# Kernel tuning notes

Hardware: AMD Instinct MI355X
Metric: run time of the kernel (lower is better)

Reference implementation:

```python
import jax, jax.numpy as jnp
import numpy as np
from jax import lax

START_IDX = 7
STOP_IDX = 8
TAGSET = 9
VOCAB = 50257
EMB = 512
HID = 1024  # bidirectional: HID//2 per direction
SEQ = 8192


def _lstm_dir(x, Wih, Whh, bih, bhh, reverse):
    # x: [T, EMB]; Wih: [4H, EMB]; Whh: [4H, H]
    H = Whh.shape[1]
    xproj = x @ Wih.T + bih  # big GEMM hoisted out of the scan: [T, 4H]

    def step(carry, xp):
        h, c = carry
        g = xp + h @ Whh.T + bhh
        i, f, gg, o = jnp.split(g, 4)
        i = jax.nn.sigmoid(i)
        f = jax.nn.sigmoid(f)
        gg = jnp.tanh(gg)
        o = jax.nn.sigmoid(o)
        c = f * c + i * gg
        h = o * jnp.tanh(c)
        return (h, c), h

    init = (jnp.zeros((H,), x.dtype), jnp.zeros((H,), x.dtype))
    _, hs = lax.scan(step, init, xproj, reverse=reverse)
    return hs  # [T, H]


def _viterbi(feats, transitions):
    # feats: [T, TAGSET]; transitions[next, prev]
    init = jnp.full((TAGSET,), -10000.0, feats.dtype).at[START_IDX].set(0.0)

    def step(fv, feat):
        scores = fv[None, :] + transitions       # [next, prev]
        bp = jnp.argmax(scores, axis=1)          # best prev per next tag
        fv_new = jnp.max(scores, axis=1) + feat
        return fv_new, bp

    fv, bptrs = lax.scan(step, init, feats)
    terminal = fv + transitions[STOP_IDX]
    best = jnp.argmax(terminal)
    path_score = terminal[best]

    def back(c, bp):
        return bp[c], c

    _, path = lax.scan(back, best, bptrs, reverse=True)  # path[t] = tag at t
    return path_score, path.astype(jnp.int32)


def setup_inputs() -> dict:
    key = jax.random.key(0)
    ks = jax.random.split(key, 13)
    H = HID // 2
    s = lambda *sh: 0.05
    inp = {
        'sentence': jax.random.randint(ks[0], (SEQ,), 0, VOCAB, dtype=jnp.int32),
        'emb': jax.random.normal(ks[1], (VOCAB + 100, EMB), jnp.float32) * 0.05,
        'Wih_f': jax.random.normal(ks[2], (4 * H, EMB), jnp.float32) * 0.05,
        'Whh_f': jax.random.normal(ks[3], (4 * H, H), jnp.float32) * 0.05,
        'bih_f': jnp.zeros((4 * H,), jnp.float32),
        'bhh_f': jnp.zeros((4 * H,), jnp.float32),
        'Wih_b': jax.random.normal(ks[4], (4 * H, EMB), jnp.float32) * 0.05,
        'Whh_b': jax.random.normal(ks[5], (4 * H, H), jnp.float32) * 0.05,
        'bih_b': jnp.zeros((4 * H,), jnp.float32),
        'bhh_b': jnp.zeros((4 * H,), jnp.float32),
        'W_out': jax.random.normal(ks[6], (TAGSET, HID), jnp.float32) * 0.05,
        'b_out': jnp.zeros((TAGSET,), jnp.float32),
    }
    trans = jax.random.normal(ks[7], (TAGSET, TAGSET), jnp.float32)
    trans = trans.at[START_IDX, :].set(-10000.0)
    trans = trans.at[:, STOP_IDX].set(-10000.0)
    inp['transitions'] = trans
    return inp


def reference(sentence, emb, Wih_f, Whh_f, bih_f, bhh_f, Wih_b, Whh_b, bih_b, bhh_b, W_out, b_out, transitions):
    x = emb[sentence]                                   # [T, EMB]
    h_f = _lstm_dir(x, Wih_f, Whh_f, bih_f, bhh_f, reverse=False)
    h_b = _lstm_dir(x, Wih_b, Whh_b, bih_b, bhh_b, reverse=True)
    lstm_out = jnp.concatenate([h_f, h_b], axis=-1)     # [T, HID]
    feats = lstm_out @ W_out.T + b_out                  # [T, TAGSET]
    score, path = _viterbi(feats, transitions)
    return score, path
```

## Files before the change

kernel.cpp:

```cpp
#include <hip/hip_runtime.h>
#include <hip/hip_bf16.h>


#define T_SEQ   8192
#define EMB     512
#define HDIM    512
#define POISON64 0x7F7F7F7F7F7F7F7Full

#define ALOAD(p)  __hip_atomic_load((p), __ATOMIC_RELAXED, __HIP_MEMORY_SCOPE_AGENT)

__global__ __launch_bounds__(256) void gemm_xproj(
    const int* __restrict__ sentence, const float* __restrict__ emb,
    const float* __restrict__ Wih_f, const float* __restrict__ Wih_b,
    const float* __restrict__ bih_f, const float* __restrict__ bhh_f,
    const float* __restrict__ bih_b, const float* __restrict__ bhh_b,
    float* __restrict__ xprojb)
{
    __shared__ float As[16][132];
    __shared__ float Bs[16][132];
    __shared__ int   srow[128];

    const int tid = threadIdx.x;
    const int bm = blockIdx.x;
    const int bn = blockIdx.y;
    const int fwd = (bn < 16);
    const float* __restrict__ W = fwd ? Wih_f : Wih_b;
    const int jbase = bn * 128 - (fwd ? 0 : 2048);

    if (tid < 128) srow[tid] = sentence[bm * 128 + tid];
    __syncthreads();

    const int lkk = tid & 15;
    const int lr  = tid >> 4;
    int sr[8];
    #pragma unroll
    for (int i = 0; i < 8; ++i) sr[i] = srow[lr * 8 + i];
    const float* wbase = W + (size_t)(jbase + lr * 8) * EMB + lkk;

    const int tx = tid & 15, ty = tid >> 4;
    float acc[8][8] = {};

    for (int kb = 0; kb < 32; ++kb) {
        const int k0 = kb * 16;
        #pragma unroll
        for (int i = 0; i < 8; ++i) {
            As[lkk][lr * 8 + i] = emb[(size_t)sr[i] * EMB + k0 + lkk];
            Bs[lkk][lr * 8 + i] = wbase[(size_t)i * EMB + k0];
        }
        __syncthreads();
        #pragma unroll
        for (int kk = 0; kk < 16; ++kk) {
            const float4 a0 = *(const float4*)&As[kk][ty * 8];
            const float4 a1 = *(const float4*)&As[kk][ty * 8 + 4];
            const float4 b0 = *(const float4*)&Bs[kk][tx * 8];
            const float4 b1 = *(const float4*)&Bs[kk][tx * 8 + 4];
            const float av[8] = {a0.x,a0.y,a0.z,a0.w,a1.x,a1.y,a1.z,a1.w};
            const float bv[8] = {b0.x,b0.y,b0.z,b0.w,b1.x,b1.y,b1.z,b1.w};
            #pragma unroll
            for (int i = 0; i < 8; ++i)
                #pragma unroll
                for (int j = 0; j < 8; ++j)
                    acc[i][j] = fmaf(av[i], bv[j], acc[i][j]);
        }
        __syncthreads();
    }

    const float* b1p = fwd ? bih_f : bih_b;
    const float* b2p = fwd ? bhh_f : bhh_b;
    float bias[8];
    #pragma unroll
    for (int j = 0; j < 8; ++j) {
        const int jj = jbase + tx * 8 + j;
        bias[j] = b1p[jj] + b2p[jj];
    }
    #pragma unroll
    for (int i = 0; i < 8; ++i) {
        const int t = bm * 128 + ty * 8 + i;
        float4* dst = (float4*)&xprojb[(size_t)t * 4096 + bn * 128 + tx * 8];
        dst[0] = make_float4(acc[i][0] + bias[0], acc[i][1] + bias[1],
                             acc[i][2] + bias[2], acc[i][3] + bias[3]);
        dst[1] = make_float4(acc[i][4] + bias[4], acc[i][5] + bias[5],
                             acc[i][6] + bias[6], acc[i][7] + bias[7]);
    }
}

__device__ __forceinline__ float fsig(float x) { return 1.0f / (1.0f + __expf(-x)); }
__device__ __forceinline__ float ftanh(float x) {
    const float e = __expf(-2.0f * fabsf(x));
    return copysignf((1.0f - e) / (1.0f + e), x);
}
__device__ __forceinline__ unsigned long long pack2(float a, float b) {
    return (unsigned long long)__float_as_uint(a) |
           ((unsigned long long)__float_as_uint(b) << 32);
}
__device__ __forceinline__ float2 unpack2(unsigned long long u) {
    return make_float2(__uint_as_float((unsigned)(u & 0xffffffffull)),
                       __uint_as_float((unsigned)(u >> 32)));
}

__global__ __launch_bounds__(256, 1) void lstm_scan(
    const float* __restrict__ xprojb,
    const float* __restrict__ Whh_f, const float* __restrict__ Whh_b,
    float* __restrict__ hseq)
{
    const int tid  = threadIdx.x;
    const int lane = tid & 63;
    const int wv   = tid >> 6;
    const int blk  = blockIdx.x;
    const int dir  = blk & 1;
    const int sub  = blk >> 1;
    const float* __restrict__ Whh = dir ? Whh_b : Whh_f;
    float* hs = hseq + (size_t)dir * T_SEQ * HDIM;

    const int jm = lane >> 4;
    const int ks = lane & 15;
    const int m  = wv * 4 + jm;

    float wr[4][32];
    #pragma unroll
    for (int g = 0; g < 4; ++g) {
        const float* src = Whh + (size_t)(g * 512 + sub * 16 + m) * 512 + ks * 32;
        #pragma unroll
        for (int i = 0; i < 8; ++i) {
            const float4 v = *(const float4*)(src + 4 * i);
            wr[g][4*i] = v.x; wr[g][4*i+1] = v.y; wr[g][4*i+2] = v.z; wr[g][4*i+3] = v.w;
        }
    }

    __shared__ __align__(16) float hsh[2][16][36];

    const bool gl = (ks == 0);
    float c_state = 0.0f;

    #pragma unroll 1
    for (int s = 0; s < T_SEQ; ++s) {
        const int t = dir ? (T_SEQ - 1 - s) : s;
        const int p = s & 1;

        float xp0 = 0.f, xp1 = 0.f, xp2 = 0.f, xp3 = 0.f;
        if (gl) {
            const float* xr = xprojb + (size_t)t * 4096 + dir * 2048 + sub * 16 + m;
            xp0 = xr[0]; xp1 = xr[512]; xp2 = xr[1024]; xp3 = xr[1536];
        }

        float2 hv2;
        if (s == 0) {
            hv2 = make_float2(0.f, 0.f);
        } else {
            const int tprev = dir ? (t + 1) : (t - 1);
            const unsigned long long* hp =
                (const unsigned long long*)(hs + (size_t)tprev * HDIM) + wv * 64 + lane;
            unsigned long long u = ALOAD(hp);
            while (u == POISON64) u = ALOAD(hp);
            hv2 = unpack2(u);
        }
        *(float2*)&hsh[p][wv * 4 + (lane >> 4)][2 * (lane & 15)] = hv2;

        asm volatile("s_waitcnt lgkmcnt(0)\n\ts_barrier" ::: "memory");
        __builtin_amdgcn_sched_barrier(0);

        float a0 = 0.f, a1 = 0.f, a2 = 0.f, a3 = 0.f;
        const float4* h4 = (const float4*)&hsh[p][ks][0];
        #pragma unroll
        for (int i = 0; i < 8; ++i) {
            const float4 hv = h4[i];
            a0 = fmaf(wr[0][4*i],   hv.x, a0); a1 = fmaf(wr[1][4*i],   hv.x, a1);
            a2 = fmaf(wr[2][4*i],   hv.x, a2); a3 = fmaf(wr[3][4*i],   hv.x, a3);
            a0 = fmaf(wr[0][4*i+1], hv.y, a0); a1 = fmaf(wr[1][4*i+1], hv.y, a1);
            a2 = fmaf(wr[2][4*i+1], hv.y, a2); a3 = fmaf(wr[3][4*i+1], hv.y, a3);
            a0 = fmaf(wr[0][4*i+2], hv.z, a0); a1 = fmaf(wr[1][4*i+2], hv.z, a1);
            a2 = fmaf(wr[2][4*i+2], hv.z, a2); a3 = fmaf(wr[3][4*i+2], hv.z, a3);
            a0 = fmaf(wr[0][4*i+3], hv.w, a0); a1 = fmaf(wr[1][4*i+3], hv.w, a1);
            a2 = fmaf(wr[2][4*i+3], hv.w, a2); a3 = fmaf(wr[3][4*i+3], hv.w, a3);
        }
        #pragma unroll
        for (int d = 1; d <= 8; d <<= 1) {
            a0 += __shfl_xor(a0, d); a1 += __shfl_xor(a1, d);
            a2 += __shfl_xor(a2, d); a3 += __shfl_xor(a3, d);
        }

        float h = 0.f;
        if (gl) {
            const float i_ = fsig(a0 + xp0);
            const float f_ = fsig(a1 + xp1);
            const float g_ = ftanh(a2 + xp2);
            const float o_ = fsig(a3 + xp3);
            c_state = fmaf(f_, c_state, i_ * g_);
            h = o_ * ftanh(c_state);
        }
        const float ha = __shfl(h, (lane * 32) & 63);
        const float hb = __shfl(h, (lane * 32 + 16) & 63);
        if (lane < 2) {
            unsigned long long* hdst =
                (unsigned long long*)(hs + (size_t)t * HDIM + sub * 16 + wv * 4) ;
            __hip_atomic_store(hdst + lane, pack2(ha, hb), __ATOMIC_RELAXED,
                               __HIP_MEMORY_SCOPE_AGENT);
        }
    }
}

__global__ __launch_bounds__(256) void feats_kernel(
    const float* __restrict__ hseq, const float* __restrict__ W_out,
    const float* __restrict__ b_out, float* __restrict__ feats)
{
    const int idx = blockIdx.x * 256 + threadIdx.x;
    if (idx >= T_SEQ * 9) return;
    const int t = idx / 9;
    const int n = idx - t * 9;
    const float4* hf = (const float4*)(hseq + (size_t)t * HDIM);
    const float4* hb = (const float4*)(hseq + (size_t)(T_SEQ + t) * HDIM);
    const float4* wf = (const float4*)(W_out + (size_t)n * 1024);
    const float4* wb = wf + 128;
    float acc = b_out[n];
    #pragma unroll 8
    for (int i = 0; i < 128; ++i) {
        const float4 a = hf[i], w = wf[i];
        acc = fmaf(a.x, w.x, acc); acc = fmaf(a.y, w.y, acc);
        acc = fmaf(a.z, w.z, acc); acc = fmaf(a.w, w.w, acc);
    }
    #pragma unroll 8
    for (int i = 0; i < 128; ++i) {
        const float4 a = hb[i], w = wb[i];
        acc = fmaf(a.x, w.x, acc); acc = fmaf(a.y, w.y, acc);
        acc = fmaf(a.z, w.z, acc); acc = fmaf(a.w, w.w, acc);
    }
    feats[idx] = acc;
}

__global__ __launch_bounds__(64) void viterbi_kernel(
    const float* __restrict__ feats, const float* __restrict__ trans,
    unsigned long long* __restrict__ bpw, float* __restrict__ out)
{
    const int lane = threadIdx.x;
    __shared__ __align__(16) float flds[1024 * 9];
    __shared__ unsigned char path_lds[T_SEQ];

    float tr[9];
    #pragma unroll
    for (int p = 0; p < 9; ++p) tr[p] = 0.f;
    float tstop = 0.f;
    if (lane < 9) {
        #pragma unroll
        for (int p = 0; p < 9; ++p) tr[p] = trans[lane * 9 + p];
        tstop = trans[8 * 9 + lane];
    }
    float fv = (lane == 7) ? 0.0f : -10000.0f;

    for (int ch = 0; ch < 8; ++ch) {
        const float4* src = (const float4*)(feats + (size_t)ch * 9216);
        #pragma unroll
        for (int i = 0; i < 36; ++i)
            ((float4*)flds)[lane + i * 64] = src[lane + i * 64];
        __syncthreads();

        for (int tt = 0; tt < 1024; ++tt) {
            const int t = ch * 1024 + tt;
            const float f0 = __shfl(fv, 0), f1 = __shfl(fv, 1), f2 = __shfl(fv, 2);
            const float f3 = __shfl(fv, 3), f4 = __shfl(fv, 4), f5 = __shfl(fv, 5);
            const float f6 = __shfl(fv, 6), f7 = __shfl(fv, 7), f8 = __shfl(fv, 8);
            const float s0 = f0 + tr[0], s1 = f1 + tr[1], s2 = f2 + tr[2];
            const float s3 = f3 + tr[3], s4 = f4 + tr[4], s5 = f5 + tr[5];
            const float s6 = f6 + tr[6], s7 = f7 + tr[7], s8 = f8 + tr[8];
            const float mx = fmaxf(fmaxf(fmaxf(fmaxf(s0, s1), fmaxf(s2, s3)),
                                         fmaxf(fmaxf(s4, s5), fmaxf(s6, s7))), s8);
            const unsigned bits =
                (s0 >= mx ? 1u : 0u)   | (s1 >= mx ? 2u : 0u)   | (s2 >= mx ? 4u : 0u) |
                (s3 >= mx ? 8u : 0u)   | (s4 >= mx ? 16u : 0u)  | (s5 >= mx ? 32u : 0u) |
                (s6 >= mx ? 64u : 0u)  | (s7 >= mx ? 128u : 0u) | (s8 >= mx ? 256u : 0u);
            const int bi = __ffs(bits) - 1;
            const float feat = (lane < 9) ? flds[tt * 9 + lane] : 0.0f;
            fv = mx + feat;
            const unsigned long long b0 = __ballot(bi & 1);
            const unsigned long long b1 = __ballot(bi & 2);
            const unsigned long long b2 = __ballot(bi & 4);
            const unsigned long long b3 = __ballot(bi & 8);
            if (lane == 0) {
                bpw[t] = (b0 & 511ull) | ((b1 & 511ull) << 9) |
                         ((b2 & 511ull) << 18) | ((b3 & 511ull) << 27);
            }
        }
        __syncthreads();
    }

    const float term = fv + tstop;
    const float t0 = __shfl(term, 0), t1 = __shfl(term, 1), t2 = __shfl(term, 2);
    const float t3 = __shfl(term, 3), t4 = __shfl(term, 4), t5 = __shfl(term, 5);
    const float t6 = __shfl(term, 6), t7 = __shfl(term, 7), t8 = __shfl(term, 8);
    const float mxt = fmaxf(fmaxf(fmaxf(fmaxf(t0, t1), fmaxf(t2, t3)),
                                  fmaxf(fmaxf(t4, t5), fmaxf(t6, t7))), t8);
    const unsigned bitst =
        (t0 >= mxt ? 1u : 0u)   | (t1 >= mxt ? 2u : 0u)   | (t2 >= mxt ? 4u : 0u) |
        (t3 >= mxt ? 8u : 0u)   | (t4 >= mxt ? 16u : 0u)  | (t5 >= mxt ? 32u : 0u) |
        (t6 >= mxt ? 64u : 0u)  | (t7 >= mxt ? 128u : 0u) | (t8 >= mxt ? 256u : 0u);
    const int best = __ffs(bitst) - 1;

    if (lane == 0) {
        out[0] = mxt;
        int c = best;
        path_lds[T_SEQ - 1] = (unsigned char)c;
        for (int thi = T_SEQ - 2; thi >= 15; thi -= 16) {
            const int tlo = thi - 15;
            unsigned long long wbuf[16];
            #pragma unroll
            for (int i = 0; i < 16; ++i) wbuf[i] = bpw[tlo + 1 + i];
            #pragma unroll
            for (int i = 15; i >= 0; --i) {
                const unsigned long long wvv = wbuf[i];
                c = (int)((wvv >> c) & 1ull) |
                    ((int)((wvv >> (9 + c)) & 1ull) << 1) |
                    ((int)((wvv >> (18 + c)) & 1ull) << 2) |
                    ((int)((wvv >> (27 + c)) & 1ull) << 3);
                path_lds[tlo + i] = (unsigned char)c;
            }
        }
        for (int t2i = 14; t2i >= 0; --t2i) {
            const unsigned long long wvv = bpw[t2i + 1];
            c = (int)((wvv >> c) & 1ull) |
                ((int)((wvv >> (9 + c)) & 1ull) << 1) |
                ((int)((wvv >> (18 + c)) & 1ull) << 2) |
                ((int)((wvv >> (27 + c)) & 1ull) << 3);
            path_lds[t2i] = (unsigned char)c;
        }
    }
    __syncthreads();
    #pragma unroll 4
    for (int i = 0; i < T_SEQ / 64; ++i) {
        const int t = i * 64 + lane;
        out[1 + t] = (float)path_lds[t];
    }
}

extern "C" void kernel_launch(void* const* d_in, const int* in_sizes, int n_in,
                              void* d_out, int out_size, void* d_ws, size_t ws_size,
                              hipStream_t stream)
{
    (void)in_sizes; (void)n_in; (void)out_size; (void)ws_size;

    const int*   sentence = (const int*)  d_in[0];
    const float* emb      = (const float*)d_in[1];
    const float* Wih_f    = (const float*)d_in[2];
    const float* Whh_f    = (const float*)d_in[3];
    const float* bih_f    = (const float*)d_in[4];
    const float* bhh_f    = (const float*)d_in[5];
    const float* Wih_b    = (const float*)d_in[6];
    const float* Whh_b    = (const float*)d_in[7];
    const float* bih_b    = (const float*)d_in[8];
    const float* bhh_b    = (const float*)d_in[9];
    const float* W_out    = (const float*)d_in[10];
    const float* b_out    = (const float*)d_in[11];
    const float* trans    = (const float*)d_in[12];

    float* ws      = (float*)d_ws;
    float* xprojb  = ws;
    float* hseq    = ws + (size_t)T_SEQ * 4096;
    float* feats   = hseq + (size_t)2 * T_SEQ * HDIM;
    unsigned long long* bpw = (unsigned long long*)(feats + (size_t)T_SEQ * 9);

    hipMemsetAsync(hseq, 0x7F, (size_t)2 * T_SEQ * HDIM * sizeof(float), stream);

    gemm_xproj<<<dim3(64, 32), 256, 0, stream>>>(
        sentence, emb, Wih_f, Wih_b, bih_f, bhh_f, bih_b, bhh_b, xprojb);

    lstm_scan<<<dim3(64), 256, 0, stream>>>(
        xprojb, Whh_f, Whh_b, hseq);

    feats_kernel<<<dim3((T_SEQ * 9 + 255) / 256), 256, 0, stream>>>(
        hseq, W_out, b_out, feats);

    viterbi_kernel<<<dim3(1), 64, 0, stream>>>(feats, trans, bpw, (float*)d_out);
}
```

Baseline: 20.02 ms.

## Restructure LSTM scan into 1024-thread blocks with LDS counter sync

The recurrent scan moves from 64 blocks of 256 threads to 32 blocks of 1024 threads. Each block now owns 32 hidden units per direction, and each lane holds a 64-element slice of one gate row, which shortens the per-lane dot product and the shuffle reduction. Only 4 of the 16 waves poll global memory for the previous hidden state. The full-block s_barrier is replaced by a monotonically increasing LDS counter that all waves spin on. The aim is to cut the number of cross-block participants and barrier cost per timestep, at the price of 16-wave spin-waiting on LDS and higher register pressure per block.

New measurement: 27.19 ms. 35.8% more time.

```diff
diff --git a/kernel.cpp b/kernel.cpp
--- a/kernel.cpp
+++ b/kernel.cpp
@@ -7,7 +7,8 @@
 #define HDIM    512
 #define POISON64 0x7F7F7F7F7F7F7F7Full
 
-#define ALOAD(p)  __hip_atomic_load((p), __ATOMIC_RELAXED, __HIP_MEMORY_SCOPE_AGENT)
+#define ALOAD(p)     __hip_atomic_load((p), __ATOMIC_RELAXED, __HIP_MEMORY_SCOPE_AGENT)
+#define ASTORE(p, v) __hip_atomic_store((p), (v), __ATOMIC_RELAXED, __HIP_MEMORY_SCOPE_AGENT)
 
 __global__ __launch_bounds__(256) void gemm_xproj(
     const int* __restrict__ sentence, const float* __restrict__ emb,
@@ -98,38 +99,43 @@
                        __uint_as_float((unsigned)(u >> 32)));
 }
 
-__global__ __launch_bounds__(256, 1) void lstm_scan(
+__global__ __launch_bounds__(1024, 4) void lstm_scan(
     const float* __restrict__ xprojb,
     const float* __restrict__ Whh_f, const float* __restrict__ Whh_b,
     float* __restrict__ hseq)
 {
     const int tid  = threadIdx.x;
     const int lane = tid & 63;
-    const int wv   = tid >> 6;
+    const int w    = tid >> 6;
     const int blk  = blockIdx.x;
     const int dir  = blk & 1;
     const int sub  = blk >> 1;
     const float* __restrict__ Whh = dir ? Whh_b : Whh_f;
     float* hs = hseq + (size_t)dir * T_SEQ * HDIM;
 
-    const int jm = lane >> 4;
-    const int ks = lane & 15;
-    const int m  = wv * 4 + jm;
-
-    float wr[4][32];
-    #pragma unroll
-    for (int g = 0; g < 4; ++g) {
-        const float* src = Whh + (size_t)(g * 512 + sub * 16 + m) * 512 + ks * 32;
-        #pragma unroll
-        for (int i = 0; i < 8; ++i) {
+    const int j  = lane >> 3;
+    const int kk = lane & 7;
+    const int g  = j >> 1;
+    const int b  = j & 1;
+    const int m  = 2 * w + b;
+
+    float wr[64];
+    {
+        const float* src = Whh + (size_t)(g * 512 + sub * 32 + m) * 512 + kk * 64;
+        #pragma unroll
+        for (int i = 0; i < 16; ++i) {
             const float4 v = *(const float4*)(src + 4 * i);
-            wr[g][4*i] = v.x; wr[g][4*i+1] = v.y; wr[g][4*i+2] = v.z; wr[g][4*i+3] = v.w;
-        }
-    }
-
-    __shared__ __align__(16) float hsh[2][16][36];
-
-    const bool gl = (ks == 0);
+            wr[4*i] = v.x; wr[4*i+1] = v.y; wr[4*i+2] = v.z; wr[4*i+3] = v.w;
+        }
+    }
+
+    __shared__ __align__(16) float hsh[2][8][68];
+    __shared__ unsigned int cnt;
+    if (tid == 0) cnt = 0u;
+    __syncthreads();
+
+    const bool poller = (w < 4);
+    const bool gl = (kk == 0) && (g == 0);
     float c_state = 0.0f;
 
     #pragma unroll 1
@@ -139,62 +145,65 @@
 
         float xp0 = 0.f, xp1 = 0.f, xp2 = 0.f, xp3 = 0.f;
         if (gl) {
-            const float* xr = xprojb + (size_t)t * 4096 + dir * 2048 + sub * 16 + m;
+            const float* xr = xprojb + (size_t)t * 4096 + dir * 2048 + sub * 32 + m;
             xp0 = xr[0]; xp1 = xr[512]; xp2 = xr[1024]; xp3 = xr[1536];
         }
 
-        float2 hv2;
-        if (s == 0) {
-            hv2 = make_float2(0.f, 0.f);
-        } else {
-            const int tprev = dir ? (t + 1) : (t - 1);
-            const unsigned long long* hp =
-                (const unsigned long long*)(hs + (size_t)tprev * HDIM) + wv * 64 + lane;
-            unsigned long long u = ALOAD(hp);
-            while (u == POISON64) u = ALOAD(hp);
-            hv2 = unpack2(u);
-        }
-        *(float2*)&hsh[p][wv * 4 + (lane >> 4)][2 * (lane & 15)] = hv2;
-
-        asm volatile("s_waitcnt lgkmcnt(0)\n\ts_barrier" ::: "memory");
-        __builtin_amdgcn_sched_barrier(0);
+        if (poller) {
+            float2 hv2;
+            if (s == 0) {
+                hv2 = make_float2(0.f, 0.f);
+            } else {
+                const int tprev = dir ? (t + 1) : (t - 1);
+                const unsigned long long* hp =
+                    (const unsigned long long*)(hs + (size_t)tprev * HDIM) + w * 64 + lane;
+                unsigned long long u = ALOAD(hp);
+                while (u == POISON64) u = ALOAD(hp);
+                hv2 = unpack2(u);
+            }
+            *(float2*)&hsh[p][w * 2 + (lane >> 5)][2 * (lane & 31)] = hv2;
+            if (lane == 0)
+                __hip_atomic_fetch_add(&cnt, 1u, __ATOMIC_RELEASE,
+                                       __HIP_MEMORY_SCOPE_WORKGROUP);
+        }
+
+        const unsigned target = 4u * (unsigned)(s + 1);
+        while (__hip_atomic_load(&cnt, __ATOMIC_ACQUIRE,
+                                 __HIP_MEMORY_SCOPE_WORKGROUP) < target) {}
 
         float a0 = 0.f, a1 = 0.f, a2 = 0.f, a3 = 0.f;
-        const float4* h4 = (const float4*)&hsh[p][ks][0];
-        #pragma unroll
-        for (int i = 0; i < 8; ++i) {
+        const float4* h4 = (const float4*)&hsh[p][kk][0];
+        #pragma unroll
+        for (int i = 0; i < 16; ++i) {
             const float4 hv = h4[i];
-            a0 = fmaf(wr[0][4*i],   hv.x, a0); a1 = fmaf(wr[1][4*i],   hv.x, a1);
-            a2 = fmaf(wr[2][4*i],   hv.x, a2); a3 = fmaf(wr[3][4*i],   hv.x, a3);
-            a0 = fmaf(wr[0][4*i+1], hv.y, a0); a1 = fmaf(wr[1][4*i+1], hv.y, a1);
-            a2 = fmaf(wr[2][4*i+1], hv.y, a2); a3 = fmaf(wr[3][4*i+1], hv.y, a3);
-            a0 = fmaf(wr[0][4*i+2], hv.z, a0); a1 = fmaf(wr[1][4*i+2], hv.z, a1);
-            a2 = fmaf(wr[2][4*i+2], hv.z, a2); a3 = fmaf(wr[3][4*i+2], hv.z, a3);
-            a0 = fmaf(wr[0][4*i+3], hv.w, a0); a1 = fmaf(wr[1][4*i+3], hv.w, a1);
-            a2 = fmaf(wr[2][4*i+3], hv.w, a2); a3 = fmaf(wr[3][4*i+3], hv.w, a3);
-        }
-        #pragma unroll
-        for (int d = 1; d <= 8; d <<= 1) {
-            a0 += __shfl_xor(a0, d); a1 += __shfl_xor(a1, d);
-            a2 += __shfl_xor(a2, d); a3 += __shfl_xor(a3, d);
-        }
+            a0 = fmaf(wr[4*i],   hv.x, a0);
+            a1 = fmaf(wr[4*i+1], hv.y, a1);
+            a2 = fmaf(wr[4*i+2], hv.z, a2);
+            a3 = fmaf(wr[4*i+3], hv.w, a3);
+        }
+        float acc = (a0 + a1) + (a2 + a3);
+        acc += __shfl_xor(acc, 1);
+        acc += __shfl_xor(acc, 2);
+        acc += __shfl_xor(acc, 4);
 
         float h = 0.f;
         if (gl) {
-            const float i_ = fsig(a0 + xp0);
-            const float f_ = fsig(a1 + xp1);
-            const float g_ = ftanh(a2 + xp2);
-            const float o_ = fsig(a3 + xp3);
+            const float si = acc;
+            const float sf = __shfl(acc, 16 + lane);
+            const float sg = __shfl(acc, 32 + lane);
+            const float so = __shfl(acc, 48 + lane);
+            const float i_ = fsig(si + xp0);
+            const float f_ = fsig(sf + xp1);
+            const float g_ = ftanh(sg + xp2);
+            const float o_ = fsig(so + xp3);
             c_state = fmaf(f_, c_state, i_ * g_);
             h = o_ * ftanh(c_state);
         }
-        const float ha = __shfl(h, (lane * 32) & 63);
-        const float hb = __shfl(h, (lane * 32 + 16) & 63);
-        if (lane < 2) {
+        const float h1 = __shfl(h, 8);
+        if (lane == 0) {
             unsigned long long* hdst =
-                (unsigned long long*)(hs + (size_t)t * HDIM + sub * 16 + wv * 4) ;
-            __hip_atomic_store(hdst + lane, pack2(ha, hb), __ATOMIC_RELAXED,
-                               __HIP_MEMORY_SCOPE_AGENT);
+                (unsigned long long*)(hs + (size_t)t * HDIM) + sub * 16 + w;
+            ASTORE(hdst, pack2(h, h1));
         }
     }
 }
@@ -361,7 +370,7 @@
     gemm_xproj<<<dim3(64, 32), 256, 0, stream>>>(
         sentence, emb, Wih_f, Wih_b, bih_f, bhh_f, bih_b, bhh_b, xprojb);
 
-    lstm_scan<<<dim3(64), 256, 0, stream>>>(
+    lstm_scan<<<dim3(32), 1024, 0, stream>>>(
         xprojb, Whh_f, Whh_b, hseq);
 
     feats_kernel<<<dim3((T_SEQ * 9 + 255) / 256), 256, 0, stream>>>(
```
